# Performance work log

Hardware: AMD Instinct MI355X
Metric: run time of the kernel (lower is better)

The kernel has to match this reference:

```python
import jax, jax.numpy as jnp
import numpy as np

NEG_INF = -1e12
BN_EPS = 1e-5
ALPHA = 0.2  # LeakyReLU negative slope


def setup_inputs() -> dict:
    key = jax.random.key(0)
    k1, k2, k3, k4 = jax.random.split(key, 4)
    N, Fin, Fout = 8192, 128, 64
    inp = jax.random.normal(k1, (N, Fin), dtype=jnp.float32)
    adj = jax.random.randint(k2, (N, N), 0, 2, dtype=jnp.int32)
    W = jax.random.normal(k3, (Fin, Fout), dtype=jnp.float32) * (1.414 / np.sqrt(Fin))
    a = jax.random.normal(k4, (2 * Fout, 1), dtype=jnp.float32) * 0.1
    bn_gamma = jnp.ones((Fout,), dtype=jnp.float32)
    bn_beta = jnp.zeros((Fout,), dtype=jnp.float32)
    bn_mean = jnp.zeros((Fout,), dtype=jnp.float32)
    bn_var = jnp.ones((Fout,), dtype=jnp.float32)
    return {"inp": inp, "adj": adj, "W": W, "a": a,
            "bn_gamma": bn_gamma, "bn_beta": bn_beta,
            "bn_mean": bn_mean, "bn_var": bn_var}


def reference(inp, adj, W, a, bn_gamma, bn_beta, bn_mean, bn_var):
    # h: [N, Fout]
    h = inp @ W
    Fout = h.shape[1]
    # Split 'a' into the two halves acting on h_i and h_j:
    # e_ij = leakyrelu(a1 . h_i + a2 . h_j)  (math-equivalent to the
    # O(N^2 * 2F) repeat/cat construction in the original code)
    a1 = a[:Fout, 0]  # [Fout]
    a2 = a[Fout:, 0]  # [Fout]
    f1 = h @ a1       # [N]
    f2 = h @ a2       # [N]
    e = jax.nn.leaky_relu(f1[:, None] + f2[None, :], negative_slope=ALPHA)  # [N, N]
    e = jnp.where(adj > 0, e, NEG_INF)
    attention = jax.nn.softmax(e, axis=1)  # row-wise softmax over neighbors
    # dropout is identity in eval mode
    h_prime = attention @ h  # [N, Fout]
    # BatchNorm1d in eval mode with running stats
    h_prime = (h_prime - bn_mean) * jax.lax.rsqrt(bn_var + BN_EPS) * bn_gamma + bn_beta
    return jax.nn.elu(h_prime)  # concat=True -> ELU
```

## Files before the change

kernel.cpp:

```cpp
#include <hip/hip_runtime.h>
#include <hip/hip_bf16.h>

#define LRALPHA 0.2f
#define NN 8192
#define FIN 128
#define FOUT 64
#define TI 16
#define TJ 128
#define NT (NN / TJ)

typedef __attribute__((ext_vector_type(4))) float f32x4;
typedef __attribute__((ext_vector_type(8))) short bf16x8;
typedef __attribute__((ext_vector_type(4))) int int4v;
typedef __attribute__((ext_vector_type(2))) int int2v;

__device__ __forceinline__ void barrier_lgkm() {
  asm volatile("s_waitcnt lgkmcnt(0)\n\ts_barrier" ::: "memory");
}

__global__ __launch_bounds__(256) void prep_kernel(
    const float* __restrict__ inp, const float* __restrict__ Wg,
    const float* __restrict__ ag, float* __restrict__ f1,
    float* __restrict__ f2, unsigned short* __restrict__ hT)
{
  __shared__ alignas(16) float WlT[FOUT][FIN + 4];
  const int t = threadIdx.x;
  for (int i = t; i < FIN * FOUT; i += 256)
    WlT[i & 63][i >> 6] = Wg[i];
  __syncthreads();

  const int lane = t & 63;
  const int row0 = blockIdx.x * 16 + (t >> 6) * 4;

  float h0 = 0.f, h1 = 0.f, h2 = 0.f, h3 = 0.f;
  for (int kk = 0; kk < FIN; kk += 4) {
    f32x4 wv = *(const f32x4*)&WlT[lane][kk];
    f32x4 r0 = *(const f32x4*)&inp[(row0 + 0) * FIN + kk];
    f32x4 r1 = *(const f32x4*)&inp[(row0 + 1) * FIN + kk];
    f32x4 r2 = *(const f32x4*)&inp[(row0 + 2) * FIN + kk];
    f32x4 r3 = *(const f32x4*)&inp[(row0 + 3) * FIN + kk];
    h0 += r0[0]*wv[0] + r0[1]*wv[1] + r0[2]*wv[2] + r0[3]*wv[3];
    h1 += r1[0]*wv[0] + r1[1]*wv[1] + r1[2]*wv[2] + r1[3]*wv[3];
    h2 += r2[0]*wv[0] + r2[1]*wv[1] + r2[2]*wv[2] + r2[3]*wv[3];
    h3 += r3[0]*wv[0] + r3[1]*wv[1] + r3[2]*wv[2] + r3[3]*wv[3];
  }

  const float a1v = ag[lane], a2v = ag[64 + lane];
  float hv[4] = {h0, h1, h2, h3};
#pragma unroll
  for (int rr = 0; rr < 4; ++rr) {
    float c1 = hv[rr] * a1v;
    float c2 = hv[rr] * a2v;
#pragma unroll
    for (int off = 32; off > 0; off >>= 1) {
      c1 += __shfl_xor(c1, off);
      c2 += __shfl_xor(c2, off);
    }
    if (lane == 0) { f1[row0 + rr] = c1; f2[row0 + rr] = c2; }
    __hip_bfloat16 hb = __float2bfloat16(hv[rr]);
    hT[lane * NN + row0 + rr] = __builtin_bit_cast(unsigned short, hb);
  }
}

__global__ __launch_bounds__(256) void f2max_kernel(
    const float* __restrict__ f2, float* __restrict__ f2m)
{
  const int t = threadIdx.x;
  float m = -1e30f;
  for (int i = t; i < NN / 4; i += 256) {
    f32x4 v = ((const f32x4*)f2)[i];
    m = fmaxf(fmaxf(m, fmaxf(v[0], v[1])), fmaxf(v[2], v[3]));
  }
#pragma unroll
  for (int off = 32; off > 0; off >>= 1)
    m = fmaxf(m, __shfl_xor(m, off));
  __shared__ float ms[4];
  if ((t & 63) == 0) ms[t >> 6] = m;
  __syncthreads();
  if (t == 0)
    f2m[0] = fmaxf(fmaxf(ms[0], ms[1]), fmaxf(ms[2], ms[3]));
}

__global__ __launch_bounds__(256, 2) void gat_main(
    const int* __restrict__ adj, const float* __restrict__ f1g,
    const float* __restrict__ f2g, const float* __restrict__ f2m,
    const unsigned short* __restrict__ hTg,
    const float* __restrict__ bng, const float* __restrict__ bnb,
    const float* __restrict__ bnm, const float* __restrict__ bnv,
    float* __restrict__ out)
{
  __shared__ alignas(16) unsigned short Pl[TI][TJ + 8];
  __shared__ alignas(16) unsigned short Hl[FOUT][TJ + 8];
  __shared__ float rs_lds[TI];

  const int t = threadIdx.x;
  const int i0 = blockIdx.x * TI;

  const int pr = t >> 4;
  const int c  = t & 15;

  const float f1v = f1g[i0 + pr];
  const float fmv = f2m[0];
  float mrow = f1v + fmv;
  mrow = mrow > 0.f ? mrow : LRALPHA * mrow;

  const int hc = t >> 2;
  const int hj = (t & 3) << 5;

  const int* adjrow = adj + (i0 + pr) * NN + c * 4;
  const unsigned short* hrow = hTg + hc * NN + hj;
  const float* f2row = f2g + c * 4;

  f32x4 acc = {0.f, 0.f, 0.f, 0.f};
  float rs = 0.f;

  const int l = t & 63;
  const int w = t >> 6;
  const int koff = (l >> 4) << 3;
  const unsigned short* pA = &Pl[l & 15][koff];
  const unsigned short* pB = &Hl[(w << 4) + (l & 15)][koff];

  int4v aA0,aA1,aB0,aB1,aC0,aC1,aD0,aD1;
  f32x4 fA0,fA1,fB0,fB1,fC0,fC1,fD0,fD1;
  int4v hA0,hA1,hA2,hA3,hB0,hB1,hB2,hB3;
  int4v hC0,hC1,hC2,hC3,hD0,hD1,hD2,hD3;

#define PREF(A0,A1,F0,F1,H0,H1,H2,H3,T)                                        \
  {                                                                            \
    const int _tn = (T) < NT ? (T) : (NT - 1);                                 \
    A0 = __builtin_nontemporal_load((const int4v*)(adjrow + _tn * TJ));        \
    A1 = __builtin_nontemporal_load((const int4v*)(adjrow + _tn * TJ + 64));   \
    F0 = *(const f32x4*)(f2row + _tn * TJ);                                    \
    F1 = *(const f32x4*)(f2row + _tn * TJ + 64);                               \
    H0 = *(const int4v*)(hrow + _tn * TJ);                                     \
    H1 = *(const int4v*)(hrow + _tn * TJ + 8);                                 \
    H2 = *(const int4v*)(hrow + _tn * TJ + 16);                                \
    H3 = *(const int4v*)(hrow + _tn * TJ + 24);                                \
  }

  PREF(aA0,aA1,fA0,fA1,hA0,hA1,hA2,hA3, 0);
  PREF(aB0,aB1,fB0,fB1,hB0,hB1,hB2,hB3, 1);
  PREF(aC0,aC1,fC0,fC1,hC0,hC1,hC2,hC3, 2);
  PREF(aD0,aD1,fD0,fD1,hD0,hD1,hD2,hD3, 3);

#define TILE_BODY(A0,A1,F0,F1,H0,H1,H2,H3,T)                                   \
  {                                                                            \
    float x0 = f1v + F0[0]; x0 = fmaxf(x0, LRALPHA * x0) - mrow;               \
    float x1 = f1v + F0[1]; x1 = fmaxf(x1, LRALPHA * x1) - mrow;               \
    float x2 = f1v + F0[2]; x2 = fmaxf(x2, LRALPHA * x2) - mrow;               \
    float x3 = f1v + F0[3]; x3 = fmaxf(x3, LRALPHA * x3) - mrow;               \
    float x4 = f1v + F1[0]; x4 = fmaxf(x4, LRALPHA * x4) - mrow;               \
    float x5 = f1v + F1[1]; x5 = fmaxf(x5, LRALPHA * x5) - mrow;               \
    float x6 = f1v + F1[2]; x6 = fmaxf(x6, LRALPHA * x6) - mrow;               \
    float x7 = f1v + F1[3]; x7 = fmaxf(x7, LRALPHA * x7) - mrow;               \
    float p0 = A0[0] > 0 ? __expf(x0) : 0.f;                                   \
    float p1 = A0[1] > 0 ? __expf(x1) : 0.f;                                   \
    float p2 = A0[2] > 0 ? __expf(x2) : 0.f;                                   \
    float p3 = A0[3] > 0 ? __expf(x3) : 0.f;                                   \
    float p4 = A1[0] > 0 ? __expf(x4) : 0.f;                                   \
    float p5 = A1[1] > 0 ? __expf(x5) : 0.f;                                   \
    float p6 = A1[2] > 0 ? __expf(x6) : 0.f;                                   \
    float p7 = A1[3] > 0 ? __expf(x7) : 0.f;                                   \
    rs += ((p0 + p1) + (p2 + p3)) + ((p4 + p5) + (p6 + p7));                   \
    unsigned short u0 = __builtin_bit_cast(unsigned short, __float2bfloat16(p0)); \
    unsigned short u1 = __builtin_bit_cast(unsigned short, __float2bfloat16(p1)); \
    unsigned short u2 = __builtin_bit_cast(unsigned short, __float2bfloat16(p2)); \
    unsigned short u3 = __builtin_bit_cast(unsigned short, __float2bfloat16(p3)); \
    unsigned short u4 = __builtin_bit_cast(unsigned short, __float2bfloat16(p4)); \
    unsigned short u5 = __builtin_bit_cast(unsigned short, __float2bfloat16(p5)); \
    unsigned short u6 = __builtin_bit_cast(unsigned short, __float2bfloat16(p6)); \
    unsigned short u7 = __builtin_bit_cast(unsigned short, __float2bfloat16(p7)); \
    int2v pw0 = {(int)u0 | ((int)u1 << 16), (int)u2 | ((int)u3 << 16)};        \
    int2v pw1 = {(int)u4 | ((int)u5 << 16), (int)u6 | ((int)u7 << 16)};        \
    *(int2v*)&Pl[pr][c * 4]      = pw0;                                        \
    *(int2v*)&Pl[pr][64 + c * 4] = pw1;                                        \
    *(int4v*)&Hl[hc][hj]      = H0;                                            \
    *(int4v*)&Hl[hc][hj + 8]  = H1;                                            \
    *(int4v*)&Hl[hc][hj + 16] = H2;                                            \
    *(int4v*)&Hl[hc][hj + 24] = H3;                                            \
    PREF(A0,A1,F0,F1,H0,H1,H2,H3, (T) + 4);                                    \
    barrier_lgkm();                                                            \
    {                                                                          \
      bf16x8 av, bv;                                                           \
      av = *(const bf16x8*)(pA);       bv = *(const bf16x8*)(pB);              \
      acc = __builtin_amdgcn_mfma_f32_16x16x32_bf16(av, bv, acc, 0, 0, 0);     \
      av = *(const bf16x8*)(pA + 32);  bv = *(const bf16x8*)(pB + 32);         \
      acc = __builtin_amdgcn_mfma_f32_16x16x32_bf16(av, bv, acc, 0, 0, 0);     \
      av = *(const bf16x8*)(pA + 64);  bv = *(const bf16x8*)(pB + 64);         \
      acc = __builtin_amdgcn_mfma_f32_16x16x32_bf16(av, bv, acc, 0, 0, 0);     \
      av = *(const bf16x8*)(pA + 96);  bv = *(const bf16x8*)(pB + 96);         \
      acc = __builtin_amdgcn_mfma_f32_16x16x32_bf16(av, bv, acc, 0, 0, 0);     \
    }                                                                          \
    barrier_lgkm();                                                            \
  }

  for (int tt = 0; tt < NT; tt += 4) {
    TILE_BODY(aA0,aA1,fA0,fA1,hA0,hA1,hA2,hA3, tt);
    TILE_BODY(aB0,aB1,fB0,fB1,hB0,hB1,hB2,hB3, tt + 1);
    TILE_BODY(aC0,aC1,fC0,fC1,hC0,hC1,hC2,hC3, tt + 2);
    TILE_BODY(aD0,aD1,fD0,fD1,hD0,hD1,hD2,hD3, tt + 3);
  }
#undef TILE_BODY
#undef PREF

  rs += __shfl_xor(rs, 1);
  rs += __shfl_xor(rs, 2);
  rs += __shfl_xor(rs, 4);
  rs += __shfl_xor(rs, 8);
  if (c == 0) rs_lds[pr] = rs;
  __syncthreads();

  const int gcol = (w << 4) + (l & 15);
  const float inv_sd = rsqrtf(bnv[gcol] + 1e-5f);
  const float ga = bng[gcol], be = bnb[gcol], mu = bnm[gcol];
  const int rbase = (l >> 4) << 2;
#pragma unroll
  for (int q = 0; q < 4; ++q) {
    float v = acc[q] / rs_lds[rbase + q];
    v = (v - mu) * inv_sd * ga + be;
    v = v > 0.f ? v : expm1f(v);
    out[(i0 + rbase + q) * FOUT + gcol] = v;
  }
}

extern "C" void kernel_launch(void* const* d_in, const int* in_sizes, int n_in,
                              void* d_out, int out_size, void* d_ws, size_t ws_size,
                              hipStream_t stream)
{
  (void)in_sizes; (void)n_in; (void)out_size; (void)ws_size;
  const float* inp = (const float*)d_in[0];
  const int*   adj = (const int*)d_in[1];
  const float* Wg  = (const float*)d_in[2];
  const float* ag  = (const float*)d_in[3];
  const float* bng = (const float*)d_in[4];
  const float* bnb = (const float*)d_in[5];
  const float* bnm = (const float*)d_in[6];
  const float* bnv = (const float*)d_in[7];
  float* out = (float*)d_out;

  char* ws = (char*)d_ws;
  unsigned short* hT = (unsigned short*)ws;
  float* f1 = (float*)(ws + (size_t)NN * FOUT * 2);
  float* f2 = f1 + NN;
  float* f2m = f2 + NN;

  prep_kernel<<<NN / 16, 256, 0, stream>>>(inp, Wg, ag, f1, f2, hT);
  f2max_kernel<<<1, 256, 0, stream>>>(f2, f2m);
  gat_main<<<NN / TI, 256, 0, stream>>>(adj, f1, f2, f2m, hT,
                                        bng, bnb, bnm, bnv, out);
}
```

Baseline: 104.5 us.

## Split j-range across waves with register-direct MFMA operands and separate reduction epilogue

The main kernel now gives each wave its own 16-row by j-chunk work item (split-K over 6 chunks), building the bf16 P fragment directly in registers and loading H fragments from global memory straight into MFMA operands. This removes LDS staging and the two block barriers per tile, and raises occupancy to 3 blocks per CU. Partial accumulators and row sums go to workspace, and a new epilogue kernel reduces them and applies the normalization, BatchNorm and ELU. The cost is extra global traffic for the partials, one more kernel launch, and redundant H loads per wave without LDS sharing.

```diff
diff --git a/kernel.cpp b/kernel.cpp
--- a/kernel.cpp
+++ b/kernel.cpp
@@ -5,18 +5,11 @@
 #define NN 8192
 #define FIN 128
 #define FOUT 64
-#define TI 16
-#define TJ 128
-#define NT (NN / TJ)
+#define NJC 6
 
 typedef __attribute__((ext_vector_type(4))) float f32x4;
 typedef __attribute__((ext_vector_type(8))) short bf16x8;
 typedef __attribute__((ext_vector_type(4))) int int4v;
-typedef __attribute__((ext_vector_type(2))) int int2v;
-
-__device__ __forceinline__ void barrier_lgkm() {
-  asm volatile("s_waitcnt lgkmcnt(0)\n\ts_barrier" ::: "memory");
-}
 
 __global__ __launch_bounds__(256) void prep_kernel(
     const float* __restrict__ inp, const float* __restrict__ Wg,
@@ -81,69 +74,68 @@
     f2m[0] = fmaxf(fmaxf(ms[0], ms[1]), fmaxf(ms[2], ms[3]));
 }
 
-__global__ __launch_bounds__(256, 2) void gat_main(
+__global__ __launch_bounds__(256, 3) void gat_pv(
     const int* __restrict__ adj, const float* __restrict__ f1g,
     const float* __restrict__ f2g, const float* __restrict__ f2m,
     const unsigned short* __restrict__ hTg,
-    const float* __restrict__ bng, const float* __restrict__ bnb,
-    const float* __restrict__ bnm, const float* __restrict__ bnv,
-    float* __restrict__ out)
-{
-  __shared__ alignas(16) unsigned short Pl[TI][TJ + 8];
-  __shared__ alignas(16) unsigned short Hl[FOUT][TJ + 8];
-  __shared__ float rs_lds[TI];
-
+    float* __restrict__ pacc, float* __restrict__ prs)
+{
   const int t = threadIdx.x;
-  const int i0 = blockIdx.x * TI;
-
-  const int pr = t >> 4;
-  const int c  = t & 15;
-
-  const float f1v = f1g[i0 + pr];
+  const int l = t & 63;
+  const int w = t >> 6;
+
+  const int item = blockIdx.x * 4 + w;
+  const int rb = item / NJC;
+  const int jc = item % NJC;
+  const int r0 = rb * 16;
+
+  const int s0 = jc * 44 - 4 * (jc > 4 ? jc - 4 : 0);
+  const int s1 = s0 + (jc < 4 ? 44 : 40);
+
+  const int row = l & 15;
+  const int grp = l >> 4;
+
+  const float f1v = f1g[r0 + row];
   const float fmv = f2m[0];
   float mrow = f1v + fmv;
-  mrow = mrow > 0.f ? mrow : LRALPHA * mrow;
-
-  const int hc = t >> 2;
-  const int hj = (t & 3) << 5;
-
-  const int* adjrow = adj + (i0 + pr) * NN + c * 4;
-  const unsigned short* hrow = hTg + hc * NN + hj;
-  const float* f2row = f2g + c * 4;
-
-  f32x4 acc = {0.f, 0.f, 0.f, 0.f};
+  mrow = fmaxf(mrow, LRALPHA * mrow);
+
+  const int* adjp = adj + (size_t)(r0 + row) * NN + grp * 8;
+  const float* f2p = f2g + grp * 8;
+  const unsigned short* hp0 = hTg + (size_t)(0 * 16 + row) * NN + grp * 8;
+  const unsigned short* hp1 = hTg + (size_t)(1 * 16 + row) * NN + grp * 8;
+  const unsigned short* hp2 = hTg + (size_t)(2 * 16 + row) * NN + grp * 8;
+  const unsigned short* hp3 = hTg + (size_t)(3 * 16 + row) * NN + grp * 8;
+
+  f32x4 acc0 = {0,0,0,0}, acc1 = {0,0,0,0}, acc2 = {0,0,0,0}, acc3 = {0,0,0,0};
   float rs = 0.f;
-
-  const int l = t & 63;
-  const int w = t >> 6;
-  const int koff = (l >> 4) << 3;
-  const unsigned short* pA = &Pl[l & 15][koff];
-  const unsigned short* pB = &Hl[(w << 4) + (l & 15)][koff];
 
   int4v aA0,aA1,aB0,aB1,aC0,aC1,aD0,aD1;
   f32x4 fA0,fA1,fB0,fB1,fC0,fC1,fD0,fD1;
-  int4v hA0,hA1,hA2,hA3,hB0,hB1,hB2,hB3;
-  int4v hC0,hC1,hC2,hC3,hD0,hD1,hD2,hD3;
-
-#define PREF(A0,A1,F0,F1,H0,H1,H2,H3,T)                                        \
-  {                                                                            \
-    const int _tn = (T) < NT ? (T) : (NT - 1);                                 \
-    A0 = __builtin_nontemporal_load((const int4v*)(adjrow + _tn * TJ));        \
-    A1 = __builtin_nontemporal_load((const int4v*)(adjrow + _tn * TJ + 64));   \
-    F0 = *(const f32x4*)(f2row + _tn * TJ);                                    \
-    F1 = *(const f32x4*)(f2row + _tn * TJ + 64);                               \
-    H0 = *(const int4v*)(hrow + _tn * TJ);                                     \
-    H1 = *(const int4v*)(hrow + _tn * TJ + 8);                                 \
-    H2 = *(const int4v*)(hrow + _tn * TJ + 16);                                \
-    H3 = *(const int4v*)(hrow + _tn * TJ + 24);                                \
-  }
-
-  PREF(aA0,aA1,fA0,fA1,hA0,hA1,hA2,hA3, 0);
-  PREF(aB0,aB1,fB0,fB1,hB0,hB1,hB2,hB3, 1);
-  PREF(aC0,aC1,fC0,fC1,hC0,hC1,hC2,hC3, 2);
-  PREF(aD0,aD1,fD0,fD1,hD0,hD1,hD2,hD3, 3);
-
-#define TILE_BODY(A0,A1,F0,F1,H0,H1,H2,H3,T)                                   \
+  bf16x8 bX0,bX1,bX2,bX3,bY0,bY1,bY2,bY3;
+
+#define PREF_AF(AJ0,AJ1,F0,F1,S)                                               \
+  { int _s = (S) > 255 ? 255 : (S);                                            \
+    AJ0 = __builtin_nontemporal_load((const int4v*)(adjp + _s * 32));          \
+    AJ1 = __builtin_nontemporal_load((const int4v*)(adjp + _s * 32 + 4));      \
+    F0 = *(const f32x4*)(f2p + _s * 32);                                       \
+    F1 = *(const f32x4*)(f2p + _s * 32 + 4); }
+
+#define PREF_BV(B0,B1,B2,B3,S)                                                 \
+  { int _s = (S) > 255 ? 255 : (S);                                            \
+    B0 = *(const bf16x8*)(hp0 + _s * 32);                                      \
+    B1 = *(const bf16x8*)(hp1 + _s * 32);                                      \
+    B2 = *(const bf16x8*)(hp2 + _s * 32);                                      \
+    B3 = *(const bf16x8*)(hp3 + _s * 32); }
+
+  PREF_AF(aA0,aA1,fA0,fA1, s0);
+  PREF_AF(aB0,aB1,fB0,fB1, s0 + 1);
+  PREF_AF(aC0,aC1,fC0,fC1, s0 + 2);
+  PREF_AF(aD0,aD1,fD0,fD1, s0 + 3);
+  PREF_BV(bX0,bX1,bX2,bX3, s0);
+  PREF_BV(bY0,bY1,bY2,bY3, s0 + 1);
+
+#define BODY(S, AJ0,AJ1,F0,F1, B0,B1,B2,B3)                                    \
   {                                                                            \
     float x0 = f1v + F0[0]; x0 = fmaxf(x0, LRALPHA * x0) - mrow;               \
     float x1 = f1v + F0[1]; x1 = fmaxf(x1, LRALPHA * x1) - mrow;               \
@@ -153,14 +145,14 @@
     float x5 = f1v + F1[1]; x5 = fmaxf(x5, LRALPHA * x5) - mrow;               \
     float x6 = f1v + F1[2]; x6 = fmaxf(x6, LRALPHA * x6) - mrow;               \
     float x7 = f1v + F1[3]; x7 = fmaxf(x7, LRALPHA * x7) - mrow;               \
-    float p0 = A0[0] > 0 ? __expf(x0) : 0.f;                                   \
-    float p1 = A0[1] > 0 ? __expf(x1) : 0.f;                                   \
-    float p2 = A0[2] > 0 ? __expf(x2) : 0.f;                                   \
-    float p3 = A0[3] > 0 ? __expf(x3) : 0.f;                                   \
-    float p4 = A1[0] > 0 ? __expf(x4) : 0.f;                                   \
-    float p5 = A1[1] > 0 ? __expf(x5) : 0.f;                                   \
-    float p6 = A1[2] > 0 ? __expf(x6) : 0.f;                                   \
-    float p7 = A1[3] > 0 ? __expf(x7) : 0.f;                                   \
+    float p0 = AJ0[0] > 0 ? __expf(x0) : 0.f;                                  \
+    float p1 = AJ0[1] > 0 ? __expf(x1) : 0.f;                                  \
+    float p2 = AJ0[2] > 0 ? __expf(x2) : 0.f;                                  \
+    float p3 = AJ0[3] > 0 ? __expf(x3) : 0.f;                                  \
+    float p4 = AJ1[0] > 0 ? __expf(x4) : 0.f;                                  \
+    float p5 = AJ1[1] > 0 ? __expf(x5) : 0.f;                                  \
+    float p6 = AJ1[2] > 0 ? __expf(x6) : 0.f;                                  \
+    float p7 = AJ1[3] > 0 ? __expf(x7) : 0.f;                                  \
     rs += ((p0 + p1) + (p2 + p3)) + ((p4 + p5) + (p6 + p7));                   \
     unsigned short u0 = __builtin_bit_cast(unsigned short, __float2bfloat16(p0)); \
     unsigned short u1 = __builtin_bit_cast(unsigned short, __float2bfloat16(p1)); \
@@ -170,57 +162,59 @@
     unsigned short u5 = __builtin_bit_cast(unsigned short, __float2bfloat16(p5)); \
     unsigned short u6 = __builtin_bit_cast(unsigned short, __float2bfloat16(p6)); \
     unsigned short u7 = __builtin_bit_cast(unsigned short, __float2bfloat16(p7)); \
-    int2v pw0 = {(int)u0 | ((int)u1 << 16), (int)u2 | ((int)u3 << 16)};        \
-    int2v pw1 = {(int)u4 | ((int)u5 << 16), (int)u6 | ((int)u7 << 16)};        \
-    *(int2v*)&Pl[pr][c * 4]      = pw0;                                        \
-    *(int2v*)&Pl[pr][64 + c * 4] = pw1;                                        \
-    *(int4v*)&Hl[hc][hj]      = H0;                                            \
-    *(int4v*)&Hl[hc][hj + 8]  = H1;                                            \
-    *(int4v*)&Hl[hc][hj + 16] = H2;                                            \
-    *(int4v*)&Hl[hc][hj + 24] = H3;                                            \
-    PREF(A0,A1,F0,F1,H0,H1,H2,H3, (T) + 4);                                    \
-    barrier_lgkm();                                                            \
-    {                                                                          \
-      bf16x8 av, bv;                                                           \
-      av = *(const bf16x8*)(pA);       bv = *(const bf16x8*)(pB);              \
-      acc = __builtin_amdgcn_mfma_f32_16x16x32_bf16(av, bv, acc, 0, 0, 0);     \
-      av = *(const bf16x8*)(pA + 32);  bv = *(const bf16x8*)(pB + 32);         \
-      acc = __builtin_amdgcn_mfma_f32_16x16x32_bf16(av, bv, acc, 0, 0, 0);     \
-      av = *(const bf16x8*)(pA + 64);  bv = *(const bf16x8*)(pB + 64);         \
-      acc = __builtin_amdgcn_mfma_f32_16x16x32_bf16(av, bv, acc, 0, 0, 0);     \
-      av = *(const bf16x8*)(pA + 96);  bv = *(const bf16x8*)(pB + 96);         \
-      acc = __builtin_amdgcn_mfma_f32_16x16x32_bf16(av, bv, acc, 0, 0, 0);     \
-    }                                                                          \
-    barrier_lgkm();                                                            \
-  }
-
-  for (int tt = 0; tt < NT; tt += 4) {
-    TILE_BODY(aA0,aA1,fA0,fA1,hA0,hA1,hA2,hA3, tt);
-    TILE_BODY(aB0,aB1,fB0,fB1,hB0,hB1,hB2,hB3, tt + 1);
-    TILE_BODY(aC0,aC1,fC0,fC1,hC0,hC1,hC2,hC3, tt + 2);
-    TILE_BODY(aD0,aD1,fD0,fD1,hD0,hD1,hD2,hD3, tt + 3);
-  }
-#undef TILE_BODY
-#undef PREF
-
-  rs += __shfl_xor(rs, 1);
-  rs += __shfl_xor(rs, 2);
-  rs += __shfl_xor(rs, 4);
-  rs += __shfl_xor(rs, 8);
-  if (c == 0) rs_lds[pr] = rs;
-  __syncthreads();
-
-  const int gcol = (w << 4) + (l & 15);
-  const float inv_sd = rsqrtf(bnv[gcol] + 1e-5f);
-  const float ga = bng[gcol], be = bnb[gcol], mu = bnm[gcol];
-  const int rbase = (l >> 4) << 2;
+    int4v pw = {(int)u0 | ((int)u1 << 16), (int)u2 | ((int)u3 << 16),          \
+                (int)u4 | ((int)u5 << 16), (int)u6 | ((int)u7 << 16)};         \
+    bf16x8 av = __builtin_bit_cast(bf16x8, pw);                                \
+    PREF_AF(AJ0,AJ1,F0,F1, (S) + 4);                                           \
+    acc0 = __builtin_amdgcn_mfma_f32_16x16x32_bf16(av, B0, acc0, 0, 0, 0);     \
+    acc1 = __builtin_amdgcn_mfma_f32_16x16x32_bf16(av, B1, acc1, 0, 0, 0);     \
+    acc2 = __builtin_amdgcn_mfma_f32_16x16x32_bf16(av, B2, acc2, 0, 0, 0);     \
+    acc3 = __builtin_amdgcn_mfma_f32_16x16x32_bf16(av, B3, acc3, 0, 0, 0);     \
+    PREF_BV(B0,B1,B2,B3, (S) + 2);                                             \
+  }
+
+  for (int s = s0; s < s1; s += 4) {
+    BODY(s,     aA0,aA1,fA0,fA1, bX0,bX1,bX2,bX3);
+    BODY(s + 1, aB0,aB1,fB0,fB1, bY0,bY1,bY2,bY3);
+    BODY(s + 2, aC0,aC1,fC0,fC1, bX0,bX1,bX2,bX3);
+    BODY(s + 3, aD0,aD1,fD0,fD1, bY0,bY1,bY2,bY3);
+  }
+#undef BODY
+#undef PREF_AF
+#undef PREF_BV
+
+  rs += __shfl_xor(rs, 16);
+  rs += __shfl_xor(rs, 32);
+  if (l < 16) prs[(size_t)jc * NN + r0 + l] = rs;
+
+  float* pa = pacc + ((size_t)jc * NN + r0 + grp * 4) * FOUT + row;
 #pragma unroll
   for (int q = 0; q < 4; ++q) {
-    float v = acc[q] / rs_lds[rbase + q];
-    v = (v - mu) * inv_sd * ga + be;
-    v = v > 0.f ? v : expm1f(v);
-    out[(i0 + rbase + q) * FOUT + gcol] = v;
-  }
+    pa[q * FOUT + 0]  = acc0[q];
+    pa[q * FOUT + 16] = acc1[q];
+    pa[q * FOUT + 32] = acc2[q];
+    pa[q * FOUT + 48] = acc3[q];
+  }
+}
+
+__global__ __launch_bounds__(256) void epilogue_kernel(
+    const float* __restrict__ pacc, const float* __restrict__ prs,
+    const float* __restrict__ bng, const float* __restrict__ bnb,
+    const float* __restrict__ bnm, const float* __restrict__ bnv,
+    float* __restrict__ out)
+{
+  const int idx = blockIdx.x * 256 + threadIdx.x;
+  const int i = idx >> 6;
+  const int c = idx & 63;
+  float s = 0.f, r = 0.f;
+#pragma unroll
+  for (int jc = 0; jc < NJC; ++jc) {
+    s += pacc[(size_t)jc * NN * FOUT + idx];
+    r += prs[(size_t)jc * NN + i];
+  }
+  float v = s / r;
+  v = (v - bnm[c]) * rsqrtf(bnv[c] + 1e-5f) * bng[c] + bnb[c];
+  out[idx] = v > 0.f ? v : expm1f(v);
 }
 
 extern "C" void kernel_launch(void* const* d_in, const int* in_sizes, int n_in,
@@ -240,12 +234,16 @@
 
   char* ws = (char*)d_ws;
   unsigned short* hT = (unsigned short*)ws;
-  float* f1 = (float*)(ws + (size_t)NN * FOUT * 2);
-  float* f2 = f1 + NN;
+  float* f1  = (float*)(ws + (size_t)NN * FOUT * 2);
+  float* f2  = f1 + NN;
   float* f2m = f2 + NN;
+  float* pacc = (float*)(ws + (size_t)2 * 1024 * 1024);
+  float* prs  = (float*)(ws + (size_t)2 * 1024 * 1024
+                           + (size_t)NJC * NN * FOUT * 4);
 
   prep_kernel<<<NN / 16, 256, 0, stream>>>(inp, Wg, ag, f1, f2, hT);
   f2max_kernel<<<1, 256, 0, stream>>>(f2, f2m);
-  gat_main<<<NN / TI, 256, 0, stream>>>(adj, f1, f2, f2m, hT,
-                                        bng, bnb, bnm, bnv, out);
-}
+  gat_pv<<<(512 * NJC) / 4, 256, 0, stream>>>(adj, f1, f2, f2m, hT, pacc, prs);
+  epilogue_kernel<<<NN * FOUT / 256, 256, 0, stream>>>(pacc, prs, bng, bnb,
+                                                       bnm, bnv, out);
+}
```

Result: slower. 188.3 us (+80.2%).

## Compress adjacency to bitmask in a separate pass and restructure main attention loop

Applied to the files above, without the earlier changes.

Adds a compress kernel that reads the int32 adjacency matrix once and writes a 1-bit-per-entry mask with wave ballots. The main kernel then reads this mask instead of the full int matrix. The main kernel is also reorganised: larger column tiles (TJ=256), a 4-deep ring of P buffers in LDS with a single barrier per tile, H operands read straight from global memory instead of staged through LDS, and occupancy raised to 4 blocks per CU. The adjacency bytes still have to be read in full by the extra kernel, so the main saving is the removed LDS staging and barriers, paid for with an extra launch and a mask round-trip through memory.

```diff
diff --git a/kernel.cpp b/kernel.cpp
--- a/kernel.cpp
+++ b/kernel.cpp
@@ -6,16 +6,39 @@
 #define FIN 128
 #define FOUT 64
 #define TI 16
-#define TJ 128
-#define NT (NN / TJ)
+#define TJ 256
+#define NTL (NN / TJ)
 
 typedef __attribute__((ext_vector_type(4))) float f32x4;
 typedef __attribute__((ext_vector_type(8))) short bf16x8;
 typedef __attribute__((ext_vector_type(4))) int int4v;
-typedef __attribute__((ext_vector_type(2))) int int2v;
 
 __device__ __forceinline__ void barrier_lgkm() {
   asm volatile("s_waitcnt lgkmcnt(0)\n\ts_barrier" ::: "memory");
+}
+
+__global__ __launch_bounds__(256) void compress_kernel(
+    const int* __restrict__ adj, unsigned long long* __restrict__ mask)
+{
+  const int l = threadIdx.x & 63;
+  const int wid = (blockIdx.x * 256 + threadIdx.x) >> 6;
+  const int nw = (gridDim.x * 256) >> 6;
+  const int nchunks = NN * (NN / 256);
+  for (int c = wid; c < nchunks; c += nw) {
+    const int* base = adj + (size_t)c * 256;
+    int a0 = __builtin_nontemporal_load(base + l);
+    int a1 = __builtin_nontemporal_load(base + 64 + l);
+    int a2 = __builtin_nontemporal_load(base + 128 + l);
+    int a3 = __builtin_nontemporal_load(base + 192 + l);
+    unsigned long long b0 = __ballot(a0 > 0);
+    unsigned long long b1 = __ballot(a1 > 0);
+    unsigned long long b2 = __ballot(a2 > 0);
+    unsigned long long b3 = __ballot(a3 > 0);
+    if (l < 4) {
+      unsigned long long v = l == 0 ? b0 : (l == 1 ? b1 : (l == 2 ? b2 : b3));
+      mask[(size_t)c * 4 + l] = v;
+    }
+  }
 }
 
 __global__ __launch_bounds__(256) void prep_kernel(
@@ -81,145 +104,132 @@
     f2m[0] = fmaxf(fmaxf(ms[0], ms[1]), fmaxf(ms[2], ms[3]));
 }
 
-__global__ __launch_bounds__(256, 2) void gat_main(
-    const int* __restrict__ adj, const float* __restrict__ f1g,
-    const float* __restrict__ f2g, const float* __restrict__ f2m,
-    const unsigned short* __restrict__ hTg,
+__global__ __launch_bounds__(256, 4) void gat_main(
+    const unsigned long long* __restrict__ mask,
+    const float* __restrict__ f1g, const float* __restrict__ f2g,
+    const float* __restrict__ f2m, const unsigned short* __restrict__ hTg,
     const float* __restrict__ bng, const float* __restrict__ bnb,
     const float* __restrict__ bnm, const float* __restrict__ bnv,
     float* __restrict__ out)
 {
-  __shared__ alignas(16) unsigned short Pl[TI][TJ + 8];
-  __shared__ alignas(16) unsigned short Hl[FOUT][TJ + 8];
+  __shared__ alignas(16) unsigned short Pl[4][TI][TJ + 8];
   __shared__ float rs_lds[TI];
 
   const int t = threadIdx.x;
-  const int i0 = blockIdx.x * TI;
-
-  const int pr = t >> 4;
-  const int c  = t & 15;
-
-  const float f1v = f1g[i0 + pr];
-  const float fmv = f2m[0];
-  float mrow = f1v + fmv;
-  mrow = mrow > 0.f ? mrow : LRALPHA * mrow;
-
-  const int hc = t >> 2;
-  const int hj = (t & 3) << 5;
-
-  const int* adjrow = adj + (i0 + pr) * NN + c * 4;
-  const unsigned short* hrow = hTg + hc * NN + hj;
-  const float* f2row = f2g + c * 4;
-
-  f32x4 acc = {0.f, 0.f, 0.f, 0.f};
-  float rs = 0.f;
-
   const int l = t & 63;
   const int w = t >> 6;
-  const int koff = (l >> 4) << 3;
-  const unsigned short* pA = &Pl[l & 15][koff];
-  const unsigned short* pB = &Hl[(w << 4) + (l & 15)][koff];
-
-  int4v aA0,aA1,aB0,aB1,aC0,aC1,aD0,aD1;
-  f32x4 fA0,fA1,fB0,fB1,fC0,fC1,fD0,fD1;
-  int4v hA0,hA1,hA2,hA3,hB0,hB1,hB2,hB3;
-  int4v hC0,hC1,hC2,hC3,hD0,hD1,hD2,hD3;
-
-#define PREF(A0,A1,F0,F1,H0,H1,H2,H3,T)                                        \
+  const int i0 = blockIdx.x * TI;
+  const int g = l >> 4;
+
+  const float fmv = f2m[0];
+  float f1q[4], mrow[4];
+#pragma unroll
+  for (int q = 0; q < 4; ++q) {
+    f1q[q] = f1g[i0 + 4 * w + q];
+    float m = f1q[q] + fmv;
+    mrow[q] = fmaxf(m, LRALPHA * m);
+  }
+
+  const unsigned long long* mrow0 = mask + ((size_t)(i0 + 4 * w + 0) * NTL) * 4 + g;
+  const unsigned long long* mrow1 = mask + ((size_t)(i0 + 4 * w + 1) * NTL) * 4 + g;
+  const unsigned long long* mrow2 = mask + ((size_t)(i0 + 4 * w + 2) * NTL) * 4 + g;
+  const unsigned long long* mrow3 = mask + ((size_t)(i0 + 4 * w + 3) * NTL) * 4 + g;
+  const int mshift = (l & 15) * 4;
+
+  const float* f2p = f2g + 4 * l;
+  const unsigned short* hp = hTg + (size_t)(w * 16 + (l & 15)) * NN + g * 8;
+  const unsigned short* pAp = &Pl[0][l & 15][g * 8];
+
+  f32x4 acc = {0.f, 0.f, 0.f, 0.f};
+  float rs0 = 0.f, rs1 = 0.f, rs2 = 0.f, rs3 = 0.f;
+
+#define PRODUCE(P, MM0, MM1, MM2, MM3, FF)                                     \
   {                                                                            \
-    const int _tn = (T) < NT ? (T) : (NT - 1);                                 \
-    A0 = __builtin_nontemporal_load((const int4v*)(adjrow + _tn * TJ));        \
-    A1 = __builtin_nontemporal_load((const int4v*)(adjrow + _tn * TJ + 64));   \
-    F0 = *(const f32x4*)(f2row + _tn * TJ);                                    \
-    F1 = *(const f32x4*)(f2row + _tn * TJ + 64);                               \
-    H0 = *(const int4v*)(hrow + _tn * TJ);                                     \
-    H1 = *(const int4v*)(hrow + _tn * TJ + 8);                                 \
-    H2 = *(const int4v*)(hrow + _tn * TJ + 16);                                \
-    H3 = *(const int4v*)(hrow + _tn * TJ + 24);                                \
-  }
-
-  PREF(aA0,aA1,fA0,fA1,hA0,hA1,hA2,hA3, 0);
-  PREF(aB0,aB1,fB0,fB1,hB0,hB1,hB2,hB3, 1);
-  PREF(aC0,aC1,fC0,fC1,hC0,hC1,hC2,hC3, 2);
-  PREF(aD0,aD1,fD0,fD1,hD0,hD1,hD2,hD3, 3);
-
-#define TILE_BODY(A0,A1,F0,F1,H0,H1,H2,H3,T)                                   \
-  {                                                                            \
-    float x0 = f1v + F0[0]; x0 = fmaxf(x0, LRALPHA * x0) - mrow;               \
-    float x1 = f1v + F0[1]; x1 = fmaxf(x1, LRALPHA * x1) - mrow;               \
-    float x2 = f1v + F0[2]; x2 = fmaxf(x2, LRALPHA * x2) - mrow;               \
-    float x3 = f1v + F0[3]; x3 = fmaxf(x3, LRALPHA * x3) - mrow;               \
-    float x4 = f1v + F1[0]; x4 = fmaxf(x4, LRALPHA * x4) - mrow;               \
-    float x5 = f1v + F1[1]; x5 = fmaxf(x5, LRALPHA * x5) - mrow;               \
-    float x6 = f1v + F1[2]; x6 = fmaxf(x6, LRALPHA * x6) - mrow;               \
-    float x7 = f1v + F1[3]; x7 = fmaxf(x7, LRALPHA * x7) - mrow;               \
-    float p0 = A0[0] > 0 ? __expf(x0) : 0.f;                                   \
-    float p1 = A0[1] > 0 ? __expf(x1) : 0.f;                                   \
-    float p2 = A0[2] > 0 ? __expf(x2) : 0.f;                                   \
-    float p3 = A0[3] > 0 ? __expf(x3) : 0.f;                                   \
-    float p4 = A1[0] > 0 ? __expf(x4) : 0.f;                                   \
-    float p5 = A1[1] > 0 ? __expf(x5) : 0.f;                                   \
-    float p6 = A1[2] > 0 ? __expf(x6) : 0.f;                                   \
-    float p7 = A1[3] > 0 ? __expf(x7) : 0.f;                                   \
-    rs += ((p0 + p1) + (p2 + p3)) + ((p4 + p5) + (p6 + p7));                   \
-    unsigned short u0 = __builtin_bit_cast(unsigned short, __float2bfloat16(p0)); \
-    unsigned short u1 = __builtin_bit_cast(unsigned short, __float2bfloat16(p1)); \
-    unsigned short u2 = __builtin_bit_cast(unsigned short, __float2bfloat16(p2)); \
-    unsigned short u3 = __builtin_bit_cast(unsigned short, __float2bfloat16(p3)); \
-    unsigned short u4 = __builtin_bit_cast(unsigned short, __float2bfloat16(p4)); \
-    unsigned short u5 = __builtin_bit_cast(unsigned short, __float2bfloat16(p5)); \
-    unsigned short u6 = __builtin_bit_cast(unsigned short, __float2bfloat16(p6)); \
-    unsigned short u7 = __builtin_bit_cast(unsigned short, __float2bfloat16(p7)); \
-    int2v pw0 = {(int)u0 | ((int)u1 << 16), (int)u2 | ((int)u3 << 16)};        \
-    int2v pw1 = {(int)u4 | ((int)u5 << 16), (int)u6 | ((int)u7 << 16)};        \
-    *(int2v*)&Pl[pr][c * 4]      = pw0;                                        \
-    *(int2v*)&Pl[pr][64 + c * 4] = pw1;                                        \
-    *(int4v*)&Hl[hc][hj]      = H0;                                            \
-    *(int4v*)&Hl[hc][hj + 8]  = H1;                                            \
-    *(int4v*)&Hl[hc][hj + 16] = H2;                                            \
-    *(int4v*)&Hl[hc][hj + 24] = H3;                                            \
-    PREF(A0,A1,F0,F1,H0,H1,H2,H3, (T) + 4);                                    \
-    barrier_lgkm();                                                            \
-    {                                                                          \
-      bf16x8 av, bv;                                                           \
-      av = *(const bf16x8*)(pA);       bv = *(const bf16x8*)(pB);              \
-      acc = __builtin_amdgcn_mfma_f32_16x16x32_bf16(av, bv, acc, 0, 0, 0);     \
-      av = *(const bf16x8*)(pA + 32);  bv = *(const bf16x8*)(pB + 32);         \
-      acc = __builtin_amdgcn_mfma_f32_16x16x32_bf16(av, bv, acc, 0, 0, 0);     \
-      av = *(const bf16x8*)(pA + 64);  bv = *(const bf16x8*)(pB + 64);         \
-      acc = __builtin_amdgcn_mfma_f32_16x16x32_bf16(av, bv, acc, 0, 0, 0);     \
-      av = *(const bf16x8*)(pA + 96);  bv = *(const bf16x8*)(pB + 96);         \
-      acc = __builtin_amdgcn_mfma_f32_16x16x32_bf16(av, bv, acc, 0, 0, 0);     \
+    unsigned n0 = (unsigned)(MM0 >> mshift) & 0xF;                             \
+    unsigned n1 = (unsigned)(MM1 >> mshift) & 0xF;                             \
+    unsigned n2 = (unsigned)(MM2 >> mshift) & 0xF;                             \
+    unsigned n3 = (unsigned)(MM3 >> mshift) & 0xF;                             \
+    _Pragma("unroll")                                                          \
+    for (int q = 0; q < 4; ++q) {                                              \
+      unsigned nib = q == 0 ? n0 : (q == 1 ? n1 : (q == 2 ? n2 : n3));         \
+      float y0 = f1q[q] + FF[0]; y0 = fmaxf(y0, LRALPHA * y0) - mrow[q];       \
+      float y1 = f1q[q] + FF[1]; y1 = fmaxf(y1, LRALPHA * y1) - mrow[q];       \
+      float y2 = f1q[q] + FF[2]; y2 = fmaxf(y2, LRALPHA * y2) - mrow[q];       \
+      float y3 = f1q[q] + FF[3]; y3 = fmaxf(y3, LRALPHA * y3) - mrow[q];       \
+      float p0 = (nib & 1u) ? __expf(y0) : 0.f;                                \
+      float p1 = (nib & 2u) ? __expf(y1) : 0.f;                                \
+      float p2 = (nib & 4u) ? __expf(y2) : 0.f;                                \
+      float p3 = (nib & 8u) ? __expf(y3) : 0.f;                                \
+      if (q == 0) rs0 += (p0 + p1) + (p2 + p3);                                \
+      if (q == 1) rs1 += (p0 + p1) + (p2 + p3);                                \
+      if (q == 2) rs2 += (p0 + p1) + (p2 + p3);                                \
+      if (q == 3) rs3 += (p0 + p1) + (p2 + p3);                                \
+      unsigned short u0 = __builtin_bit_cast(unsigned short, __float2bfloat16(p0)); \
+      unsigned short u1 = __builtin_bit_cast(unsigned short, __float2bfloat16(p1)); \
+      unsigned short u2 = __builtin_bit_cast(unsigned short, __float2bfloat16(p2)); \
+      unsigned short u3 = __builtin_bit_cast(unsigned short, __float2bfloat16(p3)); \
+      unsigned long long pk = (unsigned long long)u0 |                         \
+                              ((unsigned long long)u1 << 16) |                 \
+                              ((unsigned long long)u2 << 32) |                 \
+                              ((unsigned long long)u3 << 48);                  \
+      *(unsigned long long*)&Pl[(P) & 3][4 * w + q][4 * l] = pk;               \
     }                                                                          \
-    barrier_lgkm();                                                            \
-  }
-
-  for (int tt = 0; tt < NT; tt += 4) {
-    TILE_BODY(aA0,aA1,fA0,fA1,hA0,hA1,hA2,hA3, tt);
-    TILE_BODY(aB0,aB1,fB0,fB1,hB0,hB1,hB2,hB3, tt + 1);
-    TILE_BODY(aC0,aC1,fC0,fC1,hC0,hC1,hC2,hC3, tt + 2);
-    TILE_BODY(aD0,aD1,fD0,fD1,hD0,hD1,hD2,hD3, tt + 3);
-  }
-#undef TILE_BODY
-#undef PREF
-
-  rs += __shfl_xor(rs, 1);
-  rs += __shfl_xor(rs, 2);
-  rs += __shfl_xor(rs, 4);
-  rs += __shfl_xor(rs, 8);
-  if (c == 0) rs_lds[pr] = rs;
+  }
+
+#define LOADR(MM0, MM1, MM2, MM3, FF, P)                                       \
+  { int _p = (P) < NTL ? (P) : (NTL - 1);                                      \
+    MM0 = mrow0[_p * 4]; MM1 = mrow1[_p * 4];                                  \
+    MM2 = mrow2[_p * 4]; MM3 = mrow3[_p * 4];                                  \
+    FF = *(const f32x4*)(f2p + _p * TJ); }
+
+  unsigned long long m0, m1, m2, m3;
+  f32x4 ff;
+
+  LOADR(m0, m1, m2, m3, ff, 0);
+  PRODUCE(0, m0, m1, m2, m3, ff);
+  LOADR(m0, m1, m2, m3, ff, 1);
+  PRODUCE(1, m0, m1, m2, m3, ff);
+  LOADR(m0, m1, m2, m3, ff, 2);
+
+  for (int tt = 0; tt < NTL; ++tt) {
+    if (tt < NTL - 2) {
+      PRODUCE(tt + 2, m0, m1, m2, m3, ff);
+      LOADR(m0, m1, m2, m3, ff, tt + 3);
+    }
+    barrier_lgkm();
+    const unsigned short* pa = pAp + (size_t)(tt & 3) * TI * (TJ + 8);
+    const unsigned short* pb = hp + (size_t)tt * TJ;
+#pragma unroll
+    for (int kw = 0; kw < 8; ++kw) {
+      bf16x8 av = *(const bf16x8*)(pa + kw * 32);
+      bf16x8 bv = *(const bf16x8*)(pb + kw * 32);
+      acc = __builtin_amdgcn_mfma_f32_16x16x32_bf16(av, bv, acc, 0, 0, 0);
+    }
+  }
+#undef PRODUCE
+#undef LOADR
+
+  float rsq[4] = {rs0, rs1, rs2, rs3};
+#pragma unroll
+  for (int q = 0; q < 4; ++q) {
+    float r = rsq[q];
+#pragma unroll
+    for (int off = 32; off > 0; off >>= 1)
+      r += __shfl_xor(r, off);
+    if (l == 0) rs_lds[4 * w + q] = r;
+  }
   __syncthreads();
 
-  const int gcol = (w << 4) + (l & 15);
+  const int gcol = w * 16 + (l & 15);
   const float inv_sd = rsqrtf(bnv[gcol] + 1e-5f);
   const float ga = bng[gcol], be = bnb[gcol], mu = bnm[gcol];
-  const int rbase = (l >> 4) << 2;
+  const int rbase = g * 4;
 #pragma unroll
   for (int q = 0; q < 4; ++q) {
     float v = acc[q] / rs_lds[rbase + q];
     v = (v - mu) * inv_sd * ga + be;
     v = v > 0.f ? v : expm1f(v);
-    out[(i0 + rbase + q) * FOUT + gcol] = v;
+    out[(size_t)(i0 + rbase + q) * FOUT + gcol] = v;
   }
 }
 
@@ -240,12 +250,15 @@
 
   char* ws = (char*)d_ws;
   unsigned short* hT = (unsigned short*)ws;
-  float* f1 = (float*)(ws + (size_t)NN * FOUT * 2);
-  float* f2 = f1 + NN;
+  float* f1  = (float*)(ws + (size_t)NN * FOUT * 2);
+  float* f2  = f1 + NN;
   float* f2m = f2 + NN;
-
+  unsigned long long* mask =
+      (unsigned long long*)(ws + (size_t)2 * 1024 * 1024);
+
+  compress_kernel<<<2048, 256, 0, stream>>>(adj, mask);
   prep_kernel<<<NN / 16, 256, 0, stream>>>(inp, Wg, ag, f1, f2, hT);
   f2max_kernel<<<1, 256, 0, stream>>>(f2, f2m);
-  gat_main<<<NN / TI, 256, 0, stream>>>(adj, f1, f2, f2m, hT,
+  gat_main<<<NN / TI, 256, 0, stream>>>(mask, f1, f2, f2m, hT,
                                         bng, bnb, bnm, bnv, out);
 }
```

Measured after the change: 142.5 us. +36.3%, slower.
